# Optimization experiments

Measured on AMD Instinct MI355X. Metric: run time of the kernel, lower is better.

The kernel has to match this reference:

```python
import jax, jax.numpy as jnp
import numpy as np

PAD = 3  # 7x7 conv, padding=3 (same as nn.Conv2d(257, 1, 7, padding=3))


def setup_inputs() -> dict:
    key = jax.random.key(0)
    k1, k2, k3 = jax.random.split(key, 3)
    N, C, H, W, T = 2, 256, 16, 16, 8
    feat = jax.random.normal(k1, (N, C, H, W), dtype=jnp.float32)
    # mask_init_conv weight/bias: Conv2d(in=C+1, out=1, k=7)
    w = jax.random.normal(k2, (1, C + 1, 7, 7), dtype=jnp.float32) * 0.02
    b = jnp.zeros((1,), dtype=jnp.float32)
    # binary instance masks at level 7: [N, T, H, W]
    targets = jax.random.randint(k3, (N, T, H, W), 0, 2).astype(jnp.int32)
    return {"feat": feat, "w": w, "b": b, "targets": targets}


def reference(feat, w, b, targets):
    N, C, H, W = feat.shape
    P = H * W
    T = targets.shape[1]

    # --- init_inst_pyramid, batched over all H*W positions ---
    # each position gets the shared feature plus its own one-hot plane
    onehot = jnp.eye(P, dtype=feat.dtype).reshape(P, 1, H, W)          # [P,1,H,W]
    x = jnp.concatenate(
        [jnp.broadcast_to(feat[:, None], (N, P, C, H, W)),
         jnp.broadcast_to(onehot[None], (N, P, 1, H, W))], axis=2
    ).reshape(N * P, C + 1, H, W)
    masks = jax.lax.conv_general_dilated(
        x, w, window_strides=(1, 1), padding=[(PAD, PAD), (PAD, PAD)],
        dimension_numbers=("NCHW", "OIHW", "NCHW"))
    masks = masks.reshape(N, P, H, W) + b[0]                           # [N,P,H,W]
    m = jax.nn.sigmoid(masks)

    # --- loss_of_pyramid_7, vectorized over positions ---
    tf = targets.astype(feat.dtype)                                    # [N,T,H,W]
    areas = tf.sum(axis=(2, 3))                                        # [N,T]
    on = tf.reshape(N, T, P).transpose(0, 2, 1)                        # [N,P,T]
    cnt = on.sum(-1)                                                   # [N,P]
    # among instances active at this position, pick the smallest-area one
    masked_area = jnp.where(on > 0, areas[:, None, :], jnp.inf)        # [N,P,T]
    idx = jnp.argmin(masked_area, axis=-1)                             # [N,P]
    chosen = tf[jnp.arange(N)[:, None], idx]                           # [N,P,H,W]

    loss_pos = jnp.abs(m - chosen).mean(axis=(-2, -1))                 # [N,P]
    sum_t = tf.sum(axis=1)                                             # [N,H,W]
    loss_neg = (sum_t[:, None] * m).mean(axis=(-2, -1))                # [N,P]
    loss = jnp.where(cnt > 0, loss_pos, loss_neg).sum()
    return loss
```

## Files before the change

### kernel.cpp

```cpp
#include <hip/hip_runtime.h>
#include <math.h>

#define N_   2
#define C_   256
#define H_   16
#define W_   16
#define T_   8
#define P_   256
#define PW_  12
#define PH_  7
#define PSZ_ (PH_ * PW_)
#define MAGIC_ 0x5BD1E995u


__global__ __launch_bounds__(1024)
void fused(const float* __restrict__ feat,
           const float* __restrict__ wt,
           const float* __restrict__ bias,
           const int* __restrict__ tgt,
           float* __restrict__ ws,
           float* __restrict__ out) {
    int b = blockIdx.x;
    int tid = threadIdx.x;
    int n = b >> 6, h = (b >> 2) & 15, qx = b & 3;

    __shared__ float pl[C_ * PSZ_];
    __shared__ float wsm[C_ * 49];
    __shared__ float s_tgt[T_][P_];
    __shared__ float s_ktab[49];
    __shared__ float s_area[T_];
    __shared__ float s_st[4];
    __shared__ int   s_cnt[P_];
    __shared__ int   s_idx[P_];
    __shared__ float s_base[4];
    __shared__ float s_red[64];
    __shared__ float s_part[128];

    {
        const float4* f4 = (const float4*)(feat + (size_t)n * C_ * P_);
        #pragma unroll
        for (int k = 0; k < 6; ++k) {
            int i = tid + k * 1024;
            if (i < C_ * 21) {
                int c  = i / 21, r = i - c * 21;
                int kh = r / 3,  k4 = r - kh * 3;
                int y   = h - 3 + kh;
                int gc0 = qx * 4 - 4 + k4 * 4;
                float4 v = make_float4(0.f, 0.f, 0.f, 0.f);
                if ((unsigned)y < 16u && (unsigned)gc0 < 16u)
                    v = f4[c * 64 + y * 4 + (gc0 >> 2)];
                *(float4*)(pl + c * PSZ_ + kh * PW_ + k4 * 4) = v;
            }
        }
        const float4* w4 = (const float4*)wt;
        #pragma unroll
        for (int k = 0; k < 4; ++k) {
            int i = tid + k * 1024;
            if (i < C_ * 49 / 4) ((float4*)wsm)[i] = w4[i];
        }
        for (int i = tid; i < T_ * P_; i += 1024)
            s_tgt[0][i] = (float)tgt[n * T_ * P_ + i];
        if (tid < 49) s_ktab[tid] = wt[C_ * 49 + tid];
    }
    __syncthreads();

    int wid = tid >> 6, lane = tid & 63;

    if (wid < T_) {
        int t = wid;
        float v = s_tgt[t][lane] + s_tgt[t][lane + 64]
                + s_tgt[t][lane + 128] + s_tgt[t][lane + 192];
        #pragma unroll
        for (int off = 32; off; off >>= 1) v += __shfl_down(v, off, 64);
        if (lane == 0) s_area[t] = v;
    } else if (wid == 8 && lane < 4) {
        int gpix = h * 16 + qx * 4 + lane;
        float s = 0.f;
        #pragma unroll
        for (int t = 0; t < T_; ++t) s += s_tgt[t][gpix];
        s_st[lane] = s;
    }

    int c  = tid >> 2;
    int px = tid & 3;
    float acc = 0.f;
    {
        const float* pp = pl + c * PSZ_ + (px + 1);
        const float* wc = wsm + c * 49;
        #pragma unroll
        for (int kh = 0; kh < 7; ++kh)
            #pragma unroll
            for (int kw = 0; kw < 7; ++kw)
                acc += pp[kh * PW_ + kw] * wc[kh * 7 + kw];
    }
    #pragma unroll
    for (int off = 4; off < 64; off <<= 1) acc += __shfl_down(acc, off, 64);
    if (lane < 4) s_red[wid * 4 + lane] = acc;
    __syncthreads();

    if (tid < 4) {
        float s = 0.f;
        #pragma unroll
        for (int wv = 0; wv < 16; ++wv) s += s_red[wv * 4 + tid];
        s_base[tid] = s;
    } else if (tid >= 64 && tid < 64 + P_) {
        int p = tid - 64;
        int cnt = 0; float best = 3.402823466e38f; int idx = 0;
        #pragma unroll
        for (int t = 0; t < T_; ++t) {
            float on = s_tgt[t][p];
            cnt += (int)on;
            if (on > 0.f && s_area[t] < best) { best = s_area[t]; idx = t; }
        }
        s_cnt[p] = cnt; s_idx[p] = idx;
    }
    __syncthreads();

    float bv = bias[0];
    int p = tid >> 2;
    int gpix = h * 16 + qx * 4 + px;
    int ph = p >> 4, pw = p & 15;
    int dh = ph - h + 3, dw = pw - (qx * 4 + px) + 3;
    float kc = ((unsigned)dh < 7u && (unsigned)dw < 7u) ? s_ktab[dh * 7 + dw] : 0.f;
    float m = 1.f / (1.f + expf(-(s_base[px] + kc + bv)));
    float contrib = (s_cnt[p] > 0) ? fabsf(m - s_tgt[s_idx[p]][gpix])
                                   : s_st[px] * m;

    #pragma unroll
    for (int off = 32; off; off >>= 1) contrib += __shfl_down(contrib, off, 64);
    if (lane == 0) s_red[wid] = contrib;
    __syncthreads();

    float* slotp = ws + (size_t)b * 16;
    unsigned* slotf = (unsigned*)(slotp + 1);

    if (b != 0) {
        if (tid == 0) {
            float bsum = 0.f;
            #pragma unroll
            for (int i = 0; i < 16; ++i) bsum += s_red[i];
            bsum *= (1.0f / 256.0f);
            __hip_atomic_store(slotp, bsum, __ATOMIC_RELAXED, __HIP_MEMORY_SCOPE_AGENT);
            __hip_atomic_store(slotf, MAGIC_, __ATOMIC_RELEASE, __HIP_MEMORY_SCOPE_AGENT);
        }
        return;
    }

    if (tid == 0) {
        float bsum = 0.f;
        #pragma unroll
        for (int i = 0; i < 16; ++i) bsum += s_red[i];
        s_part[0] = bsum * (1.0f / 256.0f);
    } else if (tid < 128) {
        const float* sp = ws + (size_t)tid * 16;
        const unsigned* sf = (const unsigned*)(sp + 1);
        while (__hip_atomic_load(sf, __ATOMIC_ACQUIRE, __HIP_MEMORY_SCOPE_AGENT) != MAGIC_)
            __builtin_amdgcn_s_sleep(1);
        s_part[tid] = __hip_atomic_load(sp, __ATOMIC_RELAXED, __HIP_MEMORY_SCOPE_AGENT);
    }
    __syncthreads();
    if (tid == 0) {
        float s = 0.f;
        #pragma unroll
        for (int i = 0; i < 128; ++i) s += s_part[i];
        out[0] = s;
    } else if (tid < 128) {
        unsigned* sf = (unsigned*)(ws + (size_t)tid * 16) + 1;
        __hip_atomic_store(sf, 0u, __ATOMIC_RELAXED, __HIP_MEMORY_SCOPE_AGENT);
    }
}

extern "C" void kernel_launch(void* const* d_in, const int* in_sizes, int n_in,
                              void* d_out, int out_size, void* d_ws, size_t ws_size,
                              hipStream_t stream) {
    const float* feat = (const float*)d_in[0];
    const float* wt   = (const float*)d_in[1];
    const float* bias = (const float*)d_in[2];
    const int*   tgt  = (const int*)d_in[3];
    float* out = (float*)d_out;
    float* ws  = (float*)d_ws;

    fused<<<N_ * H_ * 4, 1024, 0, stream>>>(feat, wt, bias, tgt, ws, out);
}
```

Before: 13.74 us.

## Load conv patches and weights straight into registers, drop shared staging

Each thread now handles one channel and up to two kernel rows, loading its feature float4s and 7 weights directly from global memory into registers instead of staging a padded patch plane and the whole weight tensor in LDS. Each thread accumulates all four output pixels, which are then reduced across the wave with xor shuffles. The final 128-partial sum in block 0 also switches to a wave shuffle reduction instead of a serial loop. This removes about 130KB of shared memory and a staging pass, which may allow more blocks to overlap. The cost is more shuffle reductions and more register pressure.

New measurement: 13.53 us. About the same (-1.6%).

```diff
diff --git a/kernel.cpp b/kernel.cpp
--- a/kernel.cpp
+++ b/kernel.cpp
@@ -7,9 +7,6 @@
 #define W_   16
 #define T_   8
 #define P_   256
-#define PW_  12
-#define PH_  7
-#define PSZ_ (PH_ * PW_)
 #define MAGIC_ 0x5BD1E995u
 
 
@@ -24,8 +21,6 @@
     int tid = threadIdx.x;
     int n = b >> 6, h = (b >> 2) & 15, qx = b & 3;
 
-    __shared__ float pl[C_ * PSZ_];
-    __shared__ float wsm[C_ * 49];
     __shared__ float s_tgt[T_][P_];
     __shared__ float s_ktab[49];
     __shared__ float s_area[T_];
@@ -36,32 +31,45 @@
     __shared__ float s_red[64];
     __shared__ float s_part[128];
 
+    int c = tid >> 2, g = tid & 3;
+    int kh0 = g, kh1 = g + 4;
+
+    const float4* f4 = (const float4*)(feat + (((size_t)(n * C_ + c)) << 8));
+    float4 A0 = make_float4(0,0,0,0), A1 = A0, A2 = A0;
+    float4 B0 = A0, B1 = A0, B2 = A0;
+    int gq = qx - 1;
     {
-        const float4* f4 = (const float4*)(feat + (size_t)n * C_ * P_);
+        int y0 = h - 3 + kh0;
+        if ((unsigned)y0 < 16u) {
+            if (qx != 0) A0 = f4[(y0 << 2) + gq];
+            A1 = f4[(y0 << 2) + gq + 1];
+            if (qx != 3) A2 = f4[(y0 << 2) + gq + 2];
+        }
+        int y1 = h - 3 + kh1;
+        if (g < 3 && (unsigned)y1 < 16u) {
+            if (qx != 0) B0 = f4[(y1 << 2) + gq];
+            B1 = f4[(y1 << 2) + gq + 1];
+            if (qx != 3) B2 = f4[(y1 << 2) + gq + 2];
+        }
+    }
+    float w0[7], w1[7];
+    {
+        const float* wp0 = wt + c * 49 + kh0 * 7;
         #pragma unroll
-        for (int k = 0; k < 6; ++k) {
-            int i = tid + k * 1024;
-            if (i < C_ * 21) {
-                int c  = i / 21, r = i - c * 21;
-                int kh = r / 3,  k4 = r - kh * 3;
-                int y   = h - 3 + kh;
-                int gc0 = qx * 4 - 4 + k4 * 4;
-                float4 v = make_float4(0.f, 0.f, 0.f, 0.f);
-                if ((unsigned)y < 16u && (unsigned)gc0 < 16u)
-                    v = f4[c * 64 + y * 4 + (gc0 >> 2)];
-                *(float4*)(pl + c * PSZ_ + kh * PW_ + k4 * 4) = v;
-            }
+        for (int j = 0; j < 7; ++j) w0[j] = wp0[j];
+        if (g < 3) {
+            const float* wp1 = wt + c * 49 + kh1 * 7;
+            #pragma unroll
+            for (int j = 0; j < 7; ++j) w1[j] = wp1[j];
+        } else {
+            #pragma unroll
+            for (int j = 0; j < 7; ++j) w1[j] = 0.f;
         }
-        const float4* w4 = (const float4*)wt;
-        #pragma unroll
-        for (int k = 0; k < 4; ++k) {
-            int i = tid + k * 1024;
-            if (i < C_ * 49 / 4) ((float4*)wsm)[i] = w4[i];
-        }
-        for (int i = tid; i < T_ * P_; i += 1024)
-            s_tgt[0][i] = (float)tgt[n * T_ * P_ + i];
-        if (tid < 49) s_ktab[tid] = wt[C_ * 49 + tid];
     }
+
+    for (int i = tid; i < T_ * P_; i += 1024)
+        s_tgt[0][i] = (float)tgt[n * T_ * P_ + i];
+    if (tid < 49) s_ktab[tid] = wt[C_ * 49 + tid];
     __syncthreads();
 
     int wid = tid >> 6, lane = tid & 63;
@@ -81,21 +89,22 @@
         s_st[lane] = s;
     }
 
-    int c  = tid >> 2;
-    int px = tid & 3;
-    float acc = 0.f;
-    {
-        const float* pp = pl + c * PSZ_ + (px + 1);
-        const float* wc = wsm + c * 49;
+    float r0[12] = {A0.x,A0.y,A0.z,A0.w, A1.x,A1.y,A1.z,A1.w, A2.x,A2.y,A2.z,A2.w};
+    float r1[12] = {B0.x,B0.y,B0.z,B0.w, B1.x,B1.y,B1.z,B1.w, B2.x,B2.y,B2.z,B2.w};
+    float acc[4] = {0.f, 0.f, 0.f, 0.f};
+    #pragma unroll
+    for (int kw = 0; kw < 7; ++kw)
         #pragma unroll
-        for (int kh = 0; kh < 7; ++kh)
-            #pragma unroll
-            for (int kw = 0; kw < 7; ++kw)
-                acc += pp[kh * PW_ + kw] * wc[kh * 7 + kw];
+        for (int px = 0; px < 4; ++px)
+            acc[px] += r0[px + 1 + kw] * w0[kw] + r1[px + 1 + kw] * w1[kw];
+
+    #pragma unroll
+    for (int px = 0; px < 4; ++px) {
+        float v = acc[px];
+        #pragma unroll
+        for (int off = 1; off < 64; off <<= 1) v += __shfl_xor(v, off, 64);
+        if (lane == 0) s_red[wid * 4 + px] = v;
     }
-    #pragma unroll
-    for (int off = 4; off < 64; off <<= 1) acc += __shfl_down(acc, off, 64);
-    if (lane < 4) s_red[wid * 4 + lane] = acc;
     __syncthreads();
 
     if (tid < 4) {
@@ -117,7 +126,7 @@
     __syncthreads();
 
     float bv = bias[0];
-    int p = tid >> 2;
+    int p = tid >> 2, px = tid & 3;
     int gpix = h * 16 + qx * 4 + px;
     int ph = p >> 4, pw = p & 15;
     int dh = ph - h + 3, dw = pw - (qx * 4 + px) + 3;
@@ -159,11 +168,15 @@
         s_part[tid] = __hip_atomic_load(sp, __ATOMIC_RELAXED, __HIP_MEMORY_SCOPE_AGENT);
     }
     __syncthreads();
+    if (tid < 128) {
+        float v = s_part[tid];
+        #pragma unroll
+        for (int off = 1; off < 64; off <<= 1) v += __shfl_xor(v, off, 64);
+        if (lane == 0) s_red[32 + wid] = v;
+    }
+    __syncthreads();
     if (tid == 0) {
-        float s = 0.f;
-        #pragma unroll
-        for (int i = 0; i < 128; ++i) s += s_part[i];
-        out[0] = s;
+        out[0] = s_red[32] + s_red[33];
     } else if (tid < 128) {
         unsigned* sf = (unsigned*)(ws + (size_t)tid * 16) + 1;
         __hip_atomic_store(sf, 0u, __ATOMIC_RELAXED, __HIP_MEMORY_SCOPE_AGENT);
```
